# Optimization experiments

Hardware: AMD Instinct MI355X
Metric: run time of the kernel (lower is better)

The kernel has to match this reference:

```python
import jax, jax.numpy as jnp
import numpy as np

B, N, D, E = 4, 8192, 8, 128
SCALE = float(1.0 / np.sqrt(E))  # torch MHA scaling, n_heads=1 -> head_dim=E


def _attn_dir(X, idx, mask, Wq, Wk, Wv, ipw, ipb, ow, ob):
    # X: [B,N,E]; idx, mask: [B,N,D]. Sequence per node = [self] + padded neighbors.
    neigh = jax.vmap(lambda x, i: x[i])(X, idx)               # [B,N,D,E] gather
    seq = jnp.concatenate([X[:, :, None, :], neigh], axis=2)  # [B,N,1+D,E]
    m = jnp.concatenate([jnp.ones(mask.shape[:2] + (1,), bool), mask.astype(bool)], axis=2)
    wq, wk, wv = jnp.split(ipw, 3, axis=0)                    # torch in_proj_weight [3E,E]
    bq, bk, bv = jnp.split(ipb, 3)
    # custom pre-projections (X @ W), then torch MHA in_proj (x @ w.T + b)
    q = (X @ Wq) @ wq.T + bq                                  # [B,N,E]; only self row queried
    k = (seq @ Wk) @ wk.T + bk                                # [B,N,1+D,E]
    v = (seq @ Wv) @ wv.T + bv                                # [B,N,1+D,E]
    scores = jnp.einsum('bne,bnse->bns', q, k) * SCALE
    scores = jnp.where(m, scores, jnp.finfo(scores.dtype).min)
    w = jax.nn.softmax(scores, axis=-1)
    ctx = jnp.einsum('bns,bnse->bne', w, v)
    return ctx @ ow.T + ob                                    # MHA out_proj


def setup_inputs():
    key = jax.random.key(0)
    ks = jax.random.split(key, 26)
    f32 = jnp.float32
    inp = {
        "X": jax.random.normal(ks[0], (B, N, E), f32),
        "in_idx": jax.random.randint(ks[1], (B, N, D), 0, N, dtype=jnp.int32),
        "out_idx": jax.random.randint(ks[2], (B, N, D), 0, N, dtype=jnp.int32),
        "in_mask": jax.random.randint(ks[3], (B, N, D), 0, 2, dtype=jnp.int32),
        "out_mask": jax.random.randint(ks[4], (B, N, D), 0, 2, dtype=jnp.int32),
    }
    i = 5
    for pfx in ("in_", "out_"):
        inp[pfx + "Wq"] = jax.random.uniform(ks[i], (E, E), f32) * 0.1; i += 1
        inp[pfx + "Wk"] = jax.random.uniform(ks[i], (E, E), f32) * 0.1; i += 1
        inp[pfx + "Wv"] = jax.random.uniform(ks[i], (E, E), f32) * 0.1; i += 1
        inp[pfx + "ipw"] = jax.random.normal(ks[i], (3 * E, E), f32) * 0.05; i += 1
        inp[pfx + "ipb"] = jax.random.normal(ks[i], (3 * E,), f32) * 0.02; i += 1
        inp[pfx + "ow"] = jax.random.normal(ks[i], (E, E), f32) * 0.05; i += 1
        inp[pfx + "ob"] = jax.random.normal(ks[i], (E,), f32) * 0.02; i += 1
    inp["lin_w"] = jax.random.normal(ks[i], (E, 2 * E), f32) * 0.05; i += 1
    inp["lin_b"] = jax.random.normal(ks[i], (E,), f32) * 0.02
    return inp


def reference(X, in_idx, out_idx, in_mask, out_mask,
              in_Wq, in_Wk, in_Wv, in_ipw, in_ipb, in_ow, in_ob,
              out_Wq, out_Wk, out_Wv, out_ipw, out_ipb, out_ow, out_ob,
              lin_w, lin_b):
    a_in = _attn_dir(X, in_idx, in_mask, in_Wq, in_Wk, in_Wv, in_ipw, in_ipb, in_ow, in_ob)
    a_out = _attn_dir(X, out_idx, out_mask, out_Wq, out_Wk, out_Wv, out_ipw, out_ipb, out_ow, out_ob)
    h = jnp.concatenate([a_in, a_out], axis=-1) @ lin_w.T + lin_b  # [B,N,E]
    return jax.nn.elu(h)
```

## Files before the change

kernel.cpp:

```cpp
#include <hip/hip_runtime.h>
#include <math.h>

#define NNODE 32768
#define EE 128
constexpr float SCALE = 0.08838834764831845f;

typedef unsigned short u16;
typedef __bf16 bf16x8 __attribute__((ext_vector_type(8)));
typedef float f32x4 __attribute__((ext_vector_type(4)));

__device__ __forceinline__ u16 f2bf(float f) {
    unsigned u = __float_as_uint(f);
    u += 0x7fff + ((u >> 16) & 1);
    return (u16)(u >> 16);
}
__device__ __forceinline__ unsigned pack2bf(float lo, float hi) {
    return (unsigned)f2bf(lo) | ((unsigned)f2bf(hi) << 16);
}
__device__ __forceinline__ void unpack8(uint4 u, float* f) {
    f[0] = __uint_as_float(u.x << 16);  f[1] = __uint_as_float(u.x & 0xffff0000u);
    f[2] = __uint_as_float(u.y << 16);  f[3] = __uint_as_float(u.y & 0xffff0000u);
    f[4] = __uint_as_float(u.z << 16);  f[5] = __uint_as_float(u.z & 0xffff0000u);
    f[6] = __uint_as_float(u.w << 16);  f[7] = __uint_as_float(u.w & 0xffff0000u);
}

__device__ __forceinline__ void gl_lds16(const void* g, void* l) {
    __builtin_amdgcn_global_load_lds(
        (const __attribute__((address_space(1))) unsigned int*)(uintptr_t)g,
        (__attribute__((address_space(3))) unsigned int*)(unsigned int)(uintptr_t)l,
        16, 0, 0);
}

__global__ __launch_bounds__(256) void fuse_weights(
    const float* __restrict__ Wq_in, const float* __restrict__ Wk_in,
    const float* __restrict__ Wv_in, const float* __restrict__ ipw_in,
    const float* __restrict__ ipb_in, const float* __restrict__ ow_in,
    const float* __restrict__ ob_in,
    const float* __restrict__ Wq_out, const float* __restrict__ Wk_out,
    const float* __restrict__ Wv_out, const float* __restrict__ ipw_out,
    const float* __restrict__ ipb_out, const float* __restrict__ ow_out,
    const float* __restrict__ ob_out,
    const float* __restrict__ lin_w, const float* __restrict__ lin_b,
    u16* __restrict__ McatbT, float* __restrict__ bcat,
    u16* __restrict__ PcatbT, float* __restrict__ bh)
{
    int t = blockIdx.x * 256 + threadIdx.x;
    if (t < 98304) {
        int col = t % 768, e = t / 768;
        int dir = col / 384, rem = col % 384;
        int which = rem / 128, f = rem % 128;
        const float* W = (dir == 0)
            ? (which == 0 ? Wq_in : which == 1 ? Wk_in : Wv_in)
            : (which == 0 ? Wq_out : which == 1 ? Wk_out : Wv_out);
        const float* ipw = (dir == 0) ? ipw_in : ipw_out;
        const float* wrow = ipw + (which * EE + f) * EE;
        const float* Wrow = W + e * EE;
        float s = 0.f;
        #pragma unroll
        for (int c = 0; c < EE; c += 4) {
            float4 x = *(const float4*)&Wrow[c];
            float4 y = *(const float4*)&wrow[c];
            s = fmaf(x.x, y.x, s); s = fmaf(x.y, y.y, s);
            s = fmaf(x.z, y.z, s); s = fmaf(x.w, y.w, s);
        }
        McatbT[(size_t)col * 128 + e] = f2bf(s);
    } else if (t < 98304 + 768) {
        int col = t - 98304;
        int dir = col / 384, rem = col % 384;
        int which = rem / 128, f = rem % 128;
        const float* ipb = (dir == 0) ? ipb_in : ipb_out;
        bcat[col] = ipb[which * EE + f];
    } else if (t < 98304 + 768 + 32768) {
        int u = t - (98304 + 768);
        int e2 = u / 128, f = u % 128;
        int dir = e2 / 128, e = e2 % 128;
        const float* ow = (dir == 0) ? ow_in : ow_out;
        float s = 0.f;
        for (int c = 0; c < EE; ++c)
            s += lin_w[f * 256 + dir * 128 + c] * ow[c * EE + e];
        PcatbT[(size_t)f * 256 + e2] = f2bf(s);
    } else if (t < 98304 + 768 + 32768 + 128) {
        int f = t - (98304 + 768 + 32768);
        float s = lin_b[f];
        for (int c = 0; c < EE; ++c)
            s += ob_in[c] * lin_w[f * 256 + c] + ob_out[c] * lin_w[f * 256 + 128 + c];
        bh[f] = s;
    }
}

template<int NT>
__global__ __launch_bounds__(256) void gemm_qkv(
    const float* __restrict__ X,
    const u16* __restrict__ BT,
    const float* __restrict__ bias,
    u16* __restrict__ C)
{
    __shared__ __align__(16) u16 As[128 * 128];
    __shared__ __align__(16) u16 Bs[128 * 128];
    const int tid  = threadIdx.x;
    const int lane = tid & 63;
    const int wid  = tid >> 6;
    const int bm  = blockIdx.x * 128;
    const int bn0 = blockIdx.y * (NT * 128);
    const int wr = wid >> 1, wc = wid & 1;
    const int l15 = lane & 15, l4 = lane >> 4;

    #pragma unroll
    for (int i = 0; i < 8; ++i) {
        int c = i * 256 + tid;
        int r = c >> 4, cb = c & 15;
        const float* src = &X[(size_t)(bm + r) * 128 + cb * 8];
        float4 f0 = *(const float4*)src;
        float4 f1 = *(const float4*)(src + 4);
        uint4 pk;
        pk.x = pack2bf(f0.x, f0.y); pk.y = pack2bf(f0.z, f0.w);
        pk.z = pack2bf(f1.x, f1.y); pk.w = pack2bf(f1.z, f1.w);
        *(uint4*)&As[r * 128 + ((cb ^ (r & 7)) * 8)] = pk;
    }
    __syncthreads();
    bf16x8 a[4][4];
    #pragma unroll
    for (int ks = 0; ks < 4; ++ks)
        #pragma unroll
        for (int mr = 0; mr < 4; ++mr) {
            int r = wr * 64 + mr * 16 + l15;
            int kb = ks * 4 + l4;
            a[ks][mr] = *(const bf16x8*)((const char*)As + r * 256 + ((kb ^ (r & 7)) << 4));
        }

    #pragma unroll
    for (int nt = 0; nt < NT; ++nt) {
        int bn = bn0 + nt * 128;
        __syncthreads();
        #pragma unroll
        for (int i = 0; i < 8; ++i) {
            int c = i * 256 + tid;
            int r = c >> 4, cb = c & 15;
            gl_lds16(&BT[(size_t)(bn + r) * 128 + 8 * (cb ^ (r & 7))],
                     &Bs[(size_t)(c - lane) * 8]);
        }
        __syncthreads();

        f32x4 acc[4][4] = {};
        #pragma unroll
        for (int ks = 0; ks < 4; ++ks) {
            bf16x8 bfr[4];
            #pragma unroll
            for (int nc = 0; nc < 4; ++nc) {
                int r = wc * 64 + nc * 16 + l15;
                int kb = ks * 4 + l4;
                bfr[nc] = *(const bf16x8*)((const char*)Bs + r * 256 + ((kb ^ (r & 7)) << 4));
            }
            #pragma unroll
            for (int mr = 0; mr < 4; ++mr)
                #pragma unroll
                for (int nc = 0; nc < 4; ++nc)
                    acc[mr][nc] = __builtin_amdgcn_mfma_f32_16x16x32_bf16(
                        a[ks][mr], bfr[nc], acc[mr][nc], 0, 0, 0);
        }
        #pragma unroll
        for (int nc = 0; nc < 4; ++nc) {
            int col = bn + wc * 64 + nc * 16 + l15;
            float bv = bias[col];
            #pragma unroll
            for (int mr = 0; mr < 4; ++mr)
                #pragma unroll
                for (int j = 0; j < 4; ++j) {
                    int row = bm + wr * 64 + mr * 16 + l4 * 4 + j;
                    C[(size_t)row * 768 + col] = f2bf(acc[mr][nc][j] + bv);
                }
        }
    }
}

template<int KTOT, bool ELU_F32>
__global__ __launch_bounds__(256) void gemm_mfma(
    const u16* __restrict__ A,
    const u16* __restrict__ BT,
    const float* __restrict__ bias,
    void* __restrict__ Cout, int ldc)
{
    __shared__ __align__(16) u16 As[128 * 128];
    __shared__ __align__(16) u16 Bs[128 * 128];
    const int tid  = threadIdx.x;
    const int lane = tid & 63;
    const int wid  = tid >> 6;
    const int bm = blockIdx.x * 128;
    const int bn = blockIdx.y * 128;
    const int wr = wid >> 1, wc = wid & 1;
    const int l15 = lane & 15, l4 = lane >> 4;

    f32x4 acc[4][4] = {};

    for (int k0 = 0; k0 < KTOT; k0 += 128) {
        #pragma unroll
        for (int i = 0; i < 8; ++i) {
            int c = i * 256 + tid;
            int r = c >> 4, cb = c & 15;
            int col = k0 + 8 * (cb ^ (r & 7));
            gl_lds16(&A[(size_t)(bm + r) * KTOT + col], &As[(size_t)(c - lane) * 8]);
            gl_lds16(&BT[(size_t)(bn + r) * KTOT + col], &Bs[(size_t)(c - lane) * 8]);
        }
        __syncthreads();
        #pragma unroll
        for (int ks = 0; ks < 4; ++ks) {
            bf16x8 a[4], b[4];
            #pragma unroll
            for (int mr = 0; mr < 4; ++mr) {
                int r = wr * 64 + mr * 16 + l15;
                int kb = ks * 4 + l4;
                a[mr] = *(const bf16x8*)((const char*)As + r * 256 + ((kb ^ (r & 7)) << 4));
            }
            #pragma unroll
            for (int nc = 0; nc < 4; ++nc) {
                int r = wc * 64 + nc * 16 + l15;
                int kb = ks * 4 + l4;
                b[nc] = *(const bf16x8*)((const char*)Bs + r * 256 + ((kb ^ (r & 7)) << 4));
            }
            #pragma unroll
            for (int mr = 0; mr < 4; ++mr)
                #pragma unroll
                for (int nc = 0; nc < 4; ++nc)
                    acc[mr][nc] = __builtin_amdgcn_mfma_f32_16x16x32_bf16(
                        a[mr], b[nc], acc[mr][nc], 0, 0, 0);
        }
        __syncthreads();
    }

    #pragma unroll
    for (int nc = 0; nc < 4; ++nc) {
        int col = bn + wc * 64 + nc * 16 + l15;
        float bv = bias[col];
        #pragma unroll
        for (int mr = 0; mr < 4; ++mr) {
            #pragma unroll
            for (int j = 0; j < 4; ++j) {
                int row = bm + wr * 64 + mr * 16 + l4 * 4 + j;
                float v = acc[mr][nc][j] + bv;
                if (ELU_F32) {
                    v = v > 0.f ? v : (__expf(v) - 1.f);
                    ((float*)Cout)[(size_t)row * ldc + col] = v;
                } else {
                    ((u16*)Cout)[(size_t)row * ldc + col] = f2bf(v);
                }
            }
        }
    }
}

__global__ __launch_bounds__(256) void attn_kernel(
    const u16* __restrict__ QKV,
    const int* __restrict__ in_idx, const int* __restrict__ out_idx,
    const int* __restrict__ in_mask, const int* __restrict__ out_mask,
    u16* __restrict__ CTX)
{
    const int tid = threadIdx.x;
    const int g   = tid >> 4;
    const int l   = tid & 15;
    const int pair = blockIdx.x & 7;
    const int dir = pair & 1, b = pair >> 1;
    const int nl = ((blockIdx.x >> 3) << 4) + g;
    const int node = (b << 13) + nl;
    const int qoff = dir * 384;
    const int* idx = dir == 0 ? in_idx : out_idx;
    const int* msk = dir == 0 ? in_mask : out_mask;

    const int4 i0 = *(const int4*)&idx[(size_t)node * 8];
    const int4 i1 = *(const int4*)&idx[(size_t)node * 8 + 4];
    const int4 m0 = *(const int4*)&msk[(size_t)node * 8];
    const int4 m1 = *(const int4*)&msk[(size_t)node * 8 + 4];
    const int ii[8] = { i0.x, i0.y, i0.z, i0.w, i1.x, i1.y, i1.z, i1.w };
    const int mm[8] = { m0.x, m0.y, m0.z, m0.w, m1.x, m1.y, m1.z, m1.w };

    const u16* qrow = QKV + (size_t)node * 768 + qoff;
    const u16* nrow[8];
    #pragma unroll
    for (int s = 0; s < 8; ++s)
        nrow[s] = QKV + (size_t)((b << 13) + ii[s]) * 768 + qoff;

    uint4 qv = *(const uint4*)&qrow[l * 8];
    uint4 kv[9];
    kv[0] = *(const uint4*)&qrow[128 + l * 8];
    #pragma unroll
    for (int s = 0; s < 8; ++s)
        kv[s + 1] = *(const uint4*)&nrow[s][128 + l * 8];

    float qf[8];
    unpack8(qv, qf);
    float sc[9];
    #pragma unroll
    for (int s = 0; s < 9; ++s) {
        float kf[8];
        unpack8(kv[s], kf);
        float d = 0.f;
        #pragma unroll
        for (int j = 0; j < 8; ++j) d = fmaf(qf[j], kf[j], d);
        sc[s] = d;
    }

    uint4 vv[9];
    vv[0] = *(const uint4*)&qrow[256 + l * 8];
    #pragma unroll
    for (int s = 0; s < 8; ++s)
        vv[s + 1] = *(const uint4*)&nrow[s][256 + l * 8];

    #pragma unroll
    for (int s = 0; s < 9; ++s) {
        float x = sc[s];
        x += __shfl_xor(x, 1);
        x += __shfl_xor(x, 2);
        x += __shfl_xor(x, 4);
        x += __shfl_xor(x, 8);
        sc[s] = x * SCALE;
    }
    #pragma unroll
    for (int s = 1; s < 9; ++s)
        sc[s] = mm[s - 1] ? sc[s] : -1e30f;

    float m = sc[0];
    #pragma unroll
    for (int s = 1; s < 9; ++s) m = fmaxf(m, sc[s]);
    float w[9], wsum = 0.f;
    #pragma unroll
    for (int s = 0; s < 9; ++s) { w[s] = __expf(sc[s] - m); wsum += w[s]; }
    const float inv = 1.f / wsum;

    float acc[8] = {};
    #pragma unroll
    for (int s = 0; s < 9; ++s) {
        float vf[8];
        unpack8(vv[s], vf);
        #pragma unroll
        for (int j = 0; j < 8; ++j) acc[j] = fmaf(w[s], vf[j], acc[j]);
    }
    uint4 o;
    o.x = pack2bf(acc[0] * inv, acc[1] * inv);
    o.y = pack2bf(acc[2] * inv, acc[3] * inv);
    o.z = pack2bf(acc[4] * inv, acc[5] * inv);
    o.w = pack2bf(acc[6] * inv, acc[7] * inv);
    *(uint4*)&CTX[(size_t)node * 256 + dir * 128 + l * 8] = o;
}

extern "C" void kernel_launch(void* const* d_in, const int* in_sizes, int n_in,
                              void* d_out, int out_size, void* d_ws, size_t ws_size,
                              hipStream_t stream) {
    const float* X        = (const float*)d_in[0];
    const int*   in_idx   = (const int*)d_in[1];
    const int*   out_idx  = (const int*)d_in[2];
    const int*   in_mask  = (const int*)d_in[3];
    const int*   out_mask = (const int*)d_in[4];
    const float* Wq_in  = (const float*)d_in[5];
    const float* Wk_in  = (const float*)d_in[6];
    const float* Wv_in  = (const float*)d_in[7];
    const float* ipw_in = (const float*)d_in[8];
    const float* ipb_in = (const float*)d_in[9];
    const float* ow_in  = (const float*)d_in[10];
    const float* ob_in  = (const float*)d_in[11];
    const float* Wq_out  = (const float*)d_in[12];
    const float* Wk_out  = (const float*)d_in[13];
    const float* Wv_out  = (const float*)d_in[14];
    const float* ipw_out = (const float*)d_in[15];
    const float* ipb_out = (const float*)d_in[16];
    const float* ow_out  = (const float*)d_in[17];
    const float* ob_out  = (const float*)d_in[18];
    const float* lin_w   = (const float*)d_in[19];
    const float* lin_b   = (const float*)d_in[20];

    u16* wsu    = (u16*)d_ws;
    u16* QKVb   = wsu;
    u16* CTXb   = QKVb + (size_t)25165824;
    u16* McatbT = CTXb + (size_t)8388608;
    u16* PcatbT = McatbT + 98304;
    float* bcat = (float*)(PcatbT + 32768);
    float* bh   = bcat + 768;

    fuse_weights<<<516, 256, 0, stream>>>(
        Wq_in, Wk_in, Wv_in, ipw_in, ipb_in, ow_in, ob_in,
        Wq_out, Wk_out, Wv_out, ipw_out, ipb_out, ow_out, ob_out,
        lin_w, lin_b, McatbT, bcat, PcatbT, bh);

    gemm_qkv<6><<<dim3(256, 1), 256, 0, stream>>>(X, McatbT, bcat, QKVb);

    attn_kernel<<<4096, 256, 0, stream>>>(
        QKVb, in_idx, out_idx, in_mask, out_mask, CTXb);

    gemm_mfma<256, true><<<dim3(256, 1), 256, 0, stream>>>(
        CTXb, PcatbT, bh, (float*)d_out, 128);
}
```

Before: 72.14 us.

## Fold Q/K and V projections algebraically into weights; gather raw X in attention

Rewrites the attention so scores become (X M_qk) · x_neighbor and the context is a weighted sum of raw bf16 X rows. The value projection and output projections are folded into the final GEMM weights, and the query-bias term into a per-direction bias vector. The key bias is dropped because it shifts every score equally and cancels in the softmax. This shrinks the first GEMM from 768 to 256 output columns and cuts the per-neighbor gather from K and V rows to a single 128-wide X row. It adds two small weight-prep kernels and changes rounding behavior, since the composed weights are quantized to bf16.

```diff
diff --git a/kernel.cpp b/kernel.cpp
--- a/kernel.cpp
+++ b/kernel.cpp
@@ -2,7 +2,6 @@
 #include <math.h>
 
 #define NNODE 32768
-#define EE 128
 constexpr float SCALE = 0.08838834764831845f;
 
 typedef unsigned short u16;
@@ -23,6 +22,18 @@
     f[4] = __uint_as_float(u.z << 16);  f[5] = __uint_as_float(u.z & 0xffff0000u);
     f[6] = __uint_as_float(u.w << 16);  f[7] = __uint_as_float(u.w & 0xffff0000u);
 }
+__device__ __forceinline__ float dot128(const float* __restrict__ a,
+                                        const float* __restrict__ b) {
+    float s = 0.f;
+    #pragma unroll
+    for (int c = 0; c < 128; c += 4) {
+        float4 x = *(const float4*)&a[c];
+        float4 y = *(const float4*)&b[c];
+        s = fmaf(x.x, y.x, s); s = fmaf(x.y, y.y, s);
+        s = fmaf(x.z, y.z, s); s = fmaf(x.w, y.w, s);
+    }
+    return s;
+}
 
 __device__ __forceinline__ void gl_lds16(const void* g, void* l) {
     __builtin_amdgcn_global_load_lds(
@@ -31,69 +42,93 @@
         16, 0, 0);
 }
 
-__global__ __launch_bounds__(256) void fuse_weights(
+__global__ __launch_bounds__(256) void wprep1(
+    const float* __restrict__ ipw_in, const float* __restrict__ ipw_out,
     const float* __restrict__ Wq_in, const float* __restrict__ Wk_in,
-    const float* __restrict__ Wv_in, const float* __restrict__ ipw_in,
-    const float* __restrict__ ipb_in, const float* __restrict__ ow_in,
-    const float* __restrict__ ob_in,
+    const float* __restrict__ Wv_in,
     const float* __restrict__ Wq_out, const float* __restrict__ Wk_out,
-    const float* __restrict__ Wv_out, const float* __restrict__ ipw_out,
-    const float* __restrict__ ipb_out, const float* __restrict__ ow_out,
-    const float* __restrict__ ob_out,
-    const float* __restrict__ lin_w, const float* __restrict__ lin_b,
-    u16* __restrict__ McatbT, float* __restrict__ bcat,
-    u16* __restrict__ PcatbT, float* __restrict__ bh)
+    const float* __restrict__ Wv_out,
+    const float* __restrict__ ow_in, const float* __restrict__ ow_out,
+    const float* __restrict__ lin_w,
+    float* __restrict__ Af, float* __restrict__ Bmf,
+    float* __restrict__ Wtf, float* __restrict__ RTf)
 {
     int t = blockIdx.x * 256 + threadIdx.x;
-    if (t < 98304) {
-        int col = t % 768, e = t / 768;
-        int dir = col / 384, rem = col % 384;
-        int which = rem / 128, f = rem % 128;
-        const float* W = (dir == 0)
-            ? (which == 0 ? Wq_in : which == 1 ? Wk_in : Wv_in)
-            : (which == 0 ? Wq_out : which == 1 ? Wk_out : Wv_out);
-        const float* ipw = (dir == 0) ? ipw_in : ipw_out;
-        const float* wrow = ipw + (which * EE + f) * EE;
-        const float* Wrow = W + e * EE;
+    int i = t >> 7, j = t & 127;
+    int task = blockIdx.y, dir = task & 1, kind = task >> 1;
+    if (kind < 3) {
+        const float* ipw = dir ? ipw_out : ipw_in;
+        const float* W; const float* w; float* outp;
+        if (kind == 0)      { W = dir ? Wq_out : Wq_in; w = ipw;          outp = Af;  }
+        else if (kind == 1) { W = dir ? Wk_out : Wk_in; w = ipw + 16384;  outp = Bmf; }
+        else                { W = dir ? Wv_out : Wv_in; w = ipw + 32768;  outp = Wtf; }
+        outp[dir * 16384 + i * 128 + j] = dot128(W + i * 128, w + j * 128);
+    } else {
+        const float* ow = dir ? ow_out : ow_in;
+        const float* lw = lin_w + i * 256 + dir * 128;
         float s = 0.f;
         #pragma unroll
-        for (int c = 0; c < EE; c += 4) {
-            float4 x = *(const float4*)&Wrow[c];
-            float4 y = *(const float4*)&wrow[c];
-            s = fmaf(x.x, y.x, s); s = fmaf(x.y, y.y, s);
-            s = fmaf(x.z, y.z, s); s = fmaf(x.w, y.w, s);
-        }
-        McatbT[(size_t)col * 128 + e] = f2bf(s);
-    } else if (t < 98304 + 768) {
-        int col = t - 98304;
-        int dir = col / 384, rem = col % 384;
-        int which = rem / 128, f = rem % 128;
-        const float* ipb = (dir == 0) ? ipb_in : ipb_out;
-        bcat[col] = ipb[which * EE + f];
-    } else if (t < 98304 + 768 + 32768) {
-        int u = t - (98304 + 768);
-        int e2 = u / 128, f = u % 128;
-        int dir = e2 / 128, e = e2 % 128;
-        const float* ow = (dir == 0) ? ow_in : ow_out;
-        float s = 0.f;
-        for (int c = 0; c < EE; ++c)
-            s += lin_w[f * 256 + dir * 128 + c] * ow[c * EE + e];
-        PcatbT[(size_t)f * 256 + e2] = f2bf(s);
-    } else if (t < 98304 + 768 + 32768 + 128) {
-        int f = t - (98304 + 768 + 32768);
-        float s = lin_b[f];
-        for (int c = 0; c < EE; ++c)
-            s += ob_in[c] * lin_w[f * 256 + c] + ob_out[c] * lin_w[f * 256 + 128 + c];
-        bh[f] = s;
+        for (int e = 0; e < 128; e += 4) {
+            float4 l4 = *(const float4*)&lw[e];
+            s = fmaf(ow[e * 128 + j],       l4.x, s);
+            s = fmaf(ow[(e + 1) * 128 + j], l4.y, s);
+            s = fmaf(ow[(e + 2) * 128 + j], l4.z, s);
+            s = fmaf(ow[(e + 3) * 128 + j], l4.w, s);
+        }
+        RTf[dir * 16384 + i * 128 + j] = s;
+    }
+}
+
+__global__ __launch_bounds__(256) void wprep2(
+    const float* __restrict__ Af, const float* __restrict__ Bmf,
+    const float* __restrict__ Wtf, const float* __restrict__ RTf,
+    const float* __restrict__ ipb_in, const float* __restrict__ ipb_out,
+    const float* __restrict__ lin_w, const float* __restrict__ lin_b,
+    const float* __restrict__ ob_in, const float* __restrict__ ob_out,
+    u16* __restrict__ Bcat, u16* __restrict__ QfT,
+    float* __restrict__ ycat, float* __restrict__ bfin)
+{
+    int task = blockIdx.y;
+    int t = blockIdx.x * 256 + threadIdx.x;
+    if (task < 2) {
+        int dir = task, i = t >> 7, j = t & 127;
+        float s = dot128(Af + dir * 16384 + j * 128, Bmf + dir * 16384 + i * 128);
+        Bcat[(size_t)(dir * 128 + i) * 128 + j] = f2bf(s);
+    } else if (task < 4) {
+        int dir = task - 2, i = t >> 7, j = t & 127;
+        float s = dot128(Wtf + dir * 16384 + j * 128, RTf + dir * 16384 + i * 128);
+        QfT[(size_t)i * 256 + dir * 128 + j] = f2bf(s);
+    } else {
+        if (t < 256) {
+            int dir = t >> 7, d = t & 127;
+            const float* bq = dir ? ipb_out : ipb_in;
+            const float* rb = Bmf + dir * 16384 + d * 128;
+            float s = 0.f;
+            for (int f = 0; f < 128; ++f) s = fmaf(rb[f], bq[f], s);
+            ycat[t] = s;
+        } else if (t < 384) {
+            int g = t - 256;
+            float s = lin_b[g];
+            #pragma unroll
+            for (int dir = 0; dir < 2; ++dir) {
+                const float* bv = (dir ? ipb_out : ipb_in) + 256;
+                const float* rt = RTf + dir * 16384 + g * 128;
+                const float* ob = dir ? ob_out : ob_in;
+                const float* lw = lin_w + g * 256 + dir * 128;
+                for (int c = 0; c < 128; ++c)
+                    s += bv[c] * rt[c] + ob[c] * lw[c];
+            }
+            bfin[g] = s;
+        }
     }
 }
 
 template<int NT>
-__global__ __launch_bounds__(256) void gemm_qkv(
+__global__ __launch_bounds__(256) void gemm_y(
     const float* __restrict__ X,
     const u16* __restrict__ BT,
     const float* __restrict__ bias,
-    u16* __restrict__ C)
+    u16* __restrict__ C, u16* __restrict__ Xb)
 {
     __shared__ __align__(16) u16 As[128 * 128];
     __shared__ __align__(16) u16 Bs[128 * 128];
@@ -101,7 +136,6 @@
     const int lane = tid & 63;
     const int wid  = tid >> 6;
     const int bm  = blockIdx.x * 128;
-    const int bn0 = blockIdx.y * (NT * 128);
     const int wr = wid >> 1, wc = wid & 1;
     const int l15 = lane & 15, l4 = lane >> 4;
 
@@ -116,6 +150,7 @@
         pk.x = pack2bf(f0.x, f0.y); pk.y = pack2bf(f0.z, f0.w);
         pk.z = pack2bf(f1.x, f1.y); pk.w = pack2bf(f1.z, f1.w);
         *(uint4*)&As[r * 128 + ((cb ^ (r & 7)) * 8)] = pk;
+        *(uint4*)&Xb[(size_t)(bm + r) * 128 + cb * 8] = pk;
     }
     __syncthreads();
     bf16x8 a[4][4];
@@ -130,7 +165,7 @@
 
     #pragma unroll
     for (int nt = 0; nt < NT; ++nt) {
-        int bn = bn0 + nt * 128;
+        int bn = nt * 128;
         __syncthreads();
         #pragma unroll
         for (int i = 0; i < 8; ++i) {
@@ -167,7 +202,7 @@
                 #pragma unroll
                 for (int j = 0; j < 4; ++j) {
                     int row = bm + wr * 64 + mr * 16 + l4 * 4 + j;
-                    C[(size_t)row * 768 + col] = f2bf(acc[mr][nc][j] + bv);
+                    C[(size_t)row * 256 + col] = f2bf(acc[mr][nc][j] + bv);
                 }
         }
     }
@@ -249,10 +284,10 @@
 }
 
 __global__ __launch_bounds__(256) void attn_kernel(
-    const u16* __restrict__ QKV,
+    const u16* __restrict__ Y, const u16* __restrict__ Xb,
     const int* __restrict__ in_idx, const int* __restrict__ out_idx,
     const int* __restrict__ in_mask, const int* __restrict__ out_mask,
-    u16* __restrict__ CTX)
+    u16* __restrict__ XCTX)
 {
     const int tid = threadIdx.x;
     const int g   = tid >> 4;
@@ -261,7 +296,6 @@
     const int dir = pair & 1, b = pair >> 1;
     const int nl = ((blockIdx.x >> 3) << 4) + g;
     const int node = (b << 13) + nl;
-    const int qoff = dir * 384;
     const int* idx = dir == 0 ? in_idx : out_idx;
     const int* msk = dir == 0 ? in_mask : out_mask;
 
@@ -272,37 +306,25 @@
     const int ii[8] = { i0.x, i0.y, i0.z, i0.w, i1.x, i1.y, i1.z, i1.w };
     const int mm[8] = { m0.x, m0.y, m0.z, m0.w, m1.x, m1.y, m1.z, m1.w };
 
-    const u16* qrow = QKV + (size_t)node * 768 + qoff;
-    const u16* nrow[8];
+    uint4 yv = *(const uint4*)&Y[(size_t)node * 256 + dir * 128 + l * 8];
+    uint4 xv[9];
+    xv[0] = *(const uint4*)&Xb[(size_t)node * 128 + l * 8];
     #pragma unroll
     for (int s = 0; s < 8; ++s)
-        nrow[s] = QKV + (size_t)((b << 13) + ii[s]) * 768 + qoff;
-
-    uint4 qv = *(const uint4*)&qrow[l * 8];
-    uint4 kv[9];
-    kv[0] = *(const uint4*)&qrow[128 + l * 8];
-    #pragma unroll
-    for (int s = 0; s < 8; ++s)
-        kv[s + 1] = *(const uint4*)&nrow[s][128 + l * 8];
-
-    float qf[8];
-    unpack8(qv, qf);
+        xv[s + 1] = *(const uint4*)&Xb[(size_t)((b << 13) + ii[s]) * 128 + l * 8];
+
+    float yf[8];
+    unpack8(yv, yf);
     float sc[9];
     #pragma unroll
     for (int s = 0; s < 9; ++s) {
         float kf[8];
-        unpack8(kv[s], kf);
+        unpack8(xv[s], kf);
         float d = 0.f;
         #pragma unroll
-        for (int j = 0; j < 8; ++j) d = fmaf(qf[j], kf[j], d);
+        for (int j = 0; j < 8; ++j) d = fmaf(yf[j], kf[j], d);
         sc[s] = d;
     }
-
-    uint4 vv[9];
-    vv[0] = *(const uint4*)&qrow[256 + l * 8];
-    #pragma unroll
-    for (int s = 0; s < 8; ++s)
-        vv[s + 1] = *(const uint4*)&nrow[s][256 + l * 8];
 
     #pragma unroll
     for (int s = 0; s < 9; ++s) {
@@ -329,7 +351,7 @@
     #pragma unroll
     for (int s = 0; s < 9; ++s) {
         float vf[8];
-        unpack8(vv[s], vf);
+        unpack8(xv[s], vf);
         #pragma unroll
         for (int j = 0; j < 8; ++j) acc[j] = fmaf(w[s], vf[j], acc[j]);
     }
@@ -338,7 +360,7 @@
     o.y = pack2bf(acc[2] * inv, acc[3] * inv);
     o.z = pack2bf(acc[4] * inv, acc[5] * inv);
     o.w = pack2bf(acc[6] * inv, acc[7] * inv);
-    *(uint4*)&CTX[(size_t)node * 256 + dir * 128 + l * 8] = o;
+    *(uint4*)&XCTX[(size_t)node * 256 + dir * 128 + l * 8] = o;
 }
 
 extern "C" void kernel_launch(void* const* d_in, const int* in_sizes, int n_in,
@@ -366,24 +388,32 @@
     const float* lin_w   = (const float*)d_in[19];
     const float* lin_b   = (const float*)d_in[20];
 
-    u16* wsu    = (u16*)d_ws;
-    u16* QKVb   = wsu;
-    u16* CTXb   = QKVb + (size_t)25165824;
-    u16* McatbT = CTXb + (size_t)8388608;
-    u16* PcatbT = McatbT + 98304;
-    float* bcat = (float*)(PcatbT + 32768);
-    float* bh   = bcat + 768;
-
-    fuse_weights<<<516, 256, 0, stream>>>(
-        Wq_in, Wk_in, Wv_in, ipw_in, ipb_in, ow_in, ob_in,
-        Wq_out, Wk_out, Wv_out, ipw_out, ipb_out, ow_out, ob_out,
-        lin_w, lin_b, McatbT, bcat, PcatbT, bh);
-
-    gemm_qkv<6><<<dim3(256, 1), 256, 0, stream>>>(X, McatbT, bcat, QKVb);
+    char* wsb = (char*)d_ws;
+    u16*   Xbw  = (u16*)(wsb + 0);
+    u16*   Yw   = (u16*)(wsb + 8388608);
+    u16*   XCTX = (u16*)(wsb + 25165824);
+    u16*   Bcat = (u16*)(wsb + 41943040);
+    u16*   QfT  = (u16*)(wsb + 42008576);
+    float* Af   = (float*)(wsb + 42074112);
+    float* Bmf  = (float*)(wsb + 42205184);
+    float* Wtf  = (float*)(wsb + 42336256);
+    float* RTf  = (float*)(wsb + 42467328);
+    float* ycat = (float*)(wsb + 42598400);
+    float* bfin = (float*)(wsb + 42599424);
+
+    wprep1<<<dim3(64, 8), 256, 0, stream>>>(
+        ipw_in, ipw_out, Wq_in, Wk_in, Wv_in, Wq_out, Wk_out, Wv_out,
+        ow_in, ow_out, lin_w, Af, Bmf, Wtf, RTf);
+
+    wprep2<<<dim3(64, 5), 256, 0, stream>>>(
+        Af, Bmf, Wtf, RTf, ipb_in, ipb_out, lin_w, lin_b, ob_in, ob_out,
+        Bcat, QfT, ycat, bfin);
+
+    gemm_y<2><<<dim3(256, 1), 256, 0, stream>>>(X, Bcat, ycat, Yw, Xbw);
 
     attn_kernel<<<4096, 256, 0, stream>>>(
-        QKVb, in_idx, out_idx, in_mask, out_mask, CTXb);
+        Yw, Xbw, in_idx, out_idx, in_mask, out_mask, XCTX);
 
     gemm_mfma<256, true><<<dim3(256, 1), 256, 0, stream>>>(
-        CTXb, PcatbT, bh, (float*)d_out, 128);
-}
+        XCTX, QfT, bfin, (float*)d_out, 128);
+}
```

After: 69.06 us. 1.04x faster.
